# Kernel optimization log

Hardware: AMD Instinct MI355X
Metric: run time of the kernel (lower is better)

## Reference

```python
import jax, jax.numpy as jnp
import numpy as np

K_SIZE = 7
D_MODEL = 128
D_Q = 64
N_HEADS = 4
D_FF = 512
EPS = 1e-5


def _windows(x, k):
    # x: [N,E,H,W] -> [N,E,P,H,W]; zero-padded local k x k windows,
    # row-major over (dy,dx), matching nn.Unfold ordering.
    p = k // 2
    N, E, H, W = x.shape
    xp = jnp.pad(x, ((0, 0), (0, 0), (p, p), (p, p)))
    ws = [xp[:, :, i:i + H, j:j + W] for i in range(k) for j in range(k)]
    return jnp.stack(ws, axis=2)


def _layernorm(x, g, b):
    m = jnp.mean(x, -1, keepdims=True)
    v = jnp.var(x, -1, keepdims=True)
    return (x - m) * jax.lax.rsqrt(v + EPS) * g + b


def setup_inputs() -> dict:
    key = jax.random.key(0)
    ks = jax.random.split(key, 12)
    E, Q, F = D_MODEL, D_Q, D_FF

    def g(k, shape, s=0.02):
        return jax.random.normal(k, shape, jnp.float32) * s

    return dict(
        x=jax.random.normal(ks[0], (4, E, 64, 64), jnp.float32),
        qcoeff=jax.random.normal(ks[1], (4, Q), jnp.float32),
        wq=g(ks[2], (E, E)), bq=jnp.zeros((E,), jnp.float32),
        wk=g(ks[3], (E, E)), bk=jnp.zeros((E,), jnp.float32),
        wv=g(ks[4], (E, E)), bv=jnp.zeros((E,), jnp.float32),
        rel_bias=jnp.zeros((N_HEADS, K_SIZE * K_SIZE), jnp.float32),
        ln1_g=jnp.ones((E,), jnp.float32), ln1_b=jnp.zeros((E,), jnp.float32),
        bil_w=g(ks[5], (E, E, Q)), bil_b=jnp.zeros((E,), jnp.float32),
        ln2_g=jnp.ones((E,), jnp.float32), ln2_b=jnp.zeros((E,), jnp.float32),
        w1=g(ks[6], (F, E)), b1=jnp.zeros((F,), jnp.float32),
        w2=g(ks[7], (E, F)), b2=jnp.zeros((E,), jnp.float32),
    )


def reference(x, qcoeff, wq, bq, wk, bk, wv, bv, rel_bias, ln1_g, ln1_b,
              bil_w, bil_b, ln2_g, ln2_b, w1, b1, w2, b2):
    N, E, H, W = x.shape
    Nh = N_HEADS
    Hd = E // Nh
    P = K_SIZE * K_SIZE

    x_nhwc = jnp.transpose(x, (0, 2, 3, 1))              # [N,H,W,E]
    xn = _layernorm(x_nhwc, ln1_g, ln1_b)
    xnc = jnp.transpose(xn, (0, 3, 1, 2))                # [N,E,H,W]

    # 1x1-conv projections
    q = jnp.einsum('nchw,oc->nohw', xnc, wq) + bq[None, :, None, None]
    k = jnp.einsum('nchw,oc->nohw', xnc, wk) + bk[None, :, None, None]
    v = jnp.einsum('nchw,oc->nohw', xnc, wv) + bv[None, :, None, None]

    # local windows of K/V: [N,Nh,Hd,P,H,W]
    Kw = _windows(k, K_SIZE).reshape(N, Nh, Hd, P, H, W)
    Vw = _windows(v, K_SIZE).reshape(N, Nh, Hd, P, H, W)
    Qh = q.reshape(N, Nh, Hd, H, W)

    scores = jnp.einsum('nhdyx,nhdpyx->nhpyx', Qh, Kw)
    scores = scores + rel_bias[None, :, :, None, None]
    attn = jax.nn.softmax(scores, axis=2)                # softmax over P
    out = jnp.einsum('nhpyx,nhdpyx->nhdyx', attn, Vw).reshape(N, E, H, W)
    z0 = jnp.transpose(out, (0, 2, 3, 1))                # [N,H,W,E]

    # Bilinear(z0, qcoeff): qcoeff constant per (H,W) -> contract once per batch
    t = jnp.einsum('oiq,nq->noi', bil_w, qcoeff)         # [N,E,E]
    z1 = jnp.einsum('nhwi,noi->nhwo', z0, t) + bil_b

    z2 = z1 + x_nhwc
    z3 = _layernorm(z2, ln2_g, ln2_b)
    h1 = jax.nn.gelu(z3 @ w1.T + b1, approximate=False)  # dropout inactive (eval)
    z4 = h1 @ w2.T + b2 + z2
    return jnp.transpose(z4, (0, 3, 1, 2))               # [N,E,H,W]
```

## Files before the change

### kernel.cpp

```cpp
#include <hip/hip_runtime.h>
#include <cmath>

#define EPS 1e-5f
#define SZ 2097152

typedef __attribute__((ext_vector_type(8))) short short8;
typedef __attribute__((ext_vector_type(4))) float floatx4;

__device__ __forceinline__ float dot4(float4 a, float4 b) {
  return fmaf(a.x, b.x, fmaf(a.y, b.y, fmaf(a.z, b.z, a.w * b.w)));
}

__device__ __forceinline__ short f2bf(float f) {
  union { float f; unsigned u; } v; v.f = f;
  unsigned r = v.u + 0x7fff + ((v.u >> 16) & 1);
  return (short)(r >> 16);
}

__device__ __forceinline__ int xcd_band(int bid) {
  return (bid & 7) * 64 + (bid >> 3);
}

#define MFMA16(a, b, c) __builtin_amdgcn_mfma_f32_16x16x32_bf16(a, b, c, 0, 0, 0)

__global__ __launch_bounds__(512) void k_qkvln(const float* __restrict__ x,
    const float* __restrict__ g, const float* __restrict__ b,
    const float* __restrict__ wq, const float* __restrict__ wk,
    const float* __restrict__ wv, const float* __restrict__ bq,
    const float* __restrict__ bk, const float* __restrict__ bv,
    const float* __restrict__ w1, const float* __restrict__ w2,
    const float* __restrict__ bil_w, const float* __restrict__ qcoeff,
    float* __restrict__ xnhwc, short* __restrict__ qbf,
    short* __restrict__ kbf, short* __restrict__ vtb,
    short* __restrict__ w1bf, short* __restrict__ w2bf, short* __restrict__ tb) {
  __shared__ float tile[128 * 33];
  __shared__ float mres[32], rres[32];
  __shared__ __align__(16) short xs[32 * 136];
  __shared__ __align__(16) short ws[128 * 136];
  int tid = threadIdx.x;
  int l = xcd_band(blockIdx.x);
  int half = l & 1, ny = l >> 1;
  int n = ny >> 6, y = ny & 63;
  const float* xb = x + (size_t)n * 524288 + y * 64 + half * 32;
  for (int it = 0; it < 8; ++it) {
    int flat = it * 512 + tid;
    int c = flat >> 5, xpl = flat & 31;
    tile[c * 33 + xpl] = xb[(size_t)c * 4096 + xpl];
  }
  __syncthreads();
  {
    int pxl = tid >> 4, cl = tid & 15;
    float s = 0.f, sq = 0.f;
#pragma unroll
    for (int j = 0; j < 8; ++j) {
      float v = tile[(cl * 8 + j) * 33 + pxl];
      s += v; sq += v * v;
    }
    s += __shfl_xor(s, 1);  sq += __shfl_xor(sq, 1);
    s += __shfl_xor(s, 2);  sq += __shfl_xor(sq, 2);
    s += __shfl_xor(s, 4);  sq += __shfl_xor(sq, 4);
    s += __shfl_xor(s, 8);  sq += __shfl_xor(sq, 8);
    if (cl == 0) {
      float m = s * (1.f / 128.f);
      float var = sq * (1.f / 128.f) - m * m;
      mres[pxl] = m;
      rres[pxl] = rsqrtf(var + EPS);
    }
  }
  __syncthreads();
  size_t rowbase = (size_t)ny * 8192 + half * 4096;
  for (int it = 0; it < 8; ++it) {
    int flat = it * 512 + tid;
    int c = flat & 127, pxl = flat >> 7;
    float v = tile[c * 33 + pxl];
    xnhwc[rowbase + flat] = v;
    xs[pxl * 136 + c] = f2bf((v - mres[pxl]) * rres[pxl] * g[c] + b[c]);
  }
  __syncthreads();
  int w = tid >> 6, lane = tid & 63;
  int quad = lane >> 4, r16 = lane & 15;
  int wm = w & 1, wn = w >> 1;
  int stripl = wm * 16;
  short8 a[4];
#pragma unroll
  for (int kk = 0; kk < 4; ++kk)
    a[kk] = *(const short8*)&xs[(stripl + r16) * 136 + kk * 32 + quad * 8];
  const float* wptr[3] = {wq, wk, wv};
  const float* bptr[3] = {bq, bk, bv};
  for (int m = 0; m < 3; ++m) {
    __syncthreads();
    const float* wp = wptr[m];
    for (int i = tid; i < 2048; i += 512) {
      int e = i * 8;
      float4 v0 = *(const float4*)&wp[e];
      float4 v1 = *(const float4*)&wp[e + 4];
      short t8[8] = {f2bf(v0.x), f2bf(v0.y), f2bf(v0.z), f2bf(v0.w),
                     f2bf(v1.x), f2bf(v1.y), f2bf(v1.z), f2bf(v1.w)};
      int o = e >> 7, c = e & 127;
      *(uint4*)&ws[o * 136 + c] = *(uint4*)t8;
    }
    __syncthreads();
    const float* bb = bptr[m];
#pragma unroll
    for (int nt = 0; nt < 2; ++nt) {
      int o0 = wn * 32 + nt * 16;
      floatx4 acc = {0.f, 0.f, 0.f, 0.f};
#pragma unroll
      for (int kk = 0; kk < 4; ++kk) {
        short8 bfr = *(const short8*)&ws[(o0 + r16) * 136 + kk * 32 + quad * 8];
        acc = MFMA16(a[kk], bfr, acc);
      }
      float bv2 = bb[o0 + r16];
      if (m < 2) {
        short* dst = (m == 0) ? qbf : kbf;
#pragma unroll
        for (int r = 0; r < 4; ++r) {
          int pxl = stripl + quad * 4 + r;
          dst[rowbase + pxl * 128 + o0 + r16] = f2bf(acc[r] + bv2);
        }
      } else {
        short t4[4] = {f2bf(acc[0] + bv2), f2bf(acc[1] + bv2),
                       f2bf(acc[2] + bv2), f2bf(acc[3] + bv2)};
        *(uint2*)&vtb[(size_t)(n * 128 + o0 + r16) * 4096 + y * 64 + half * 32 +
                      stripl + quad * 4] = *(uint2*)t4;
      }
    }
  }
  int gtid = blockIdx.x * 512 + tid;
  if (gtid < 8192) {
    int e = gtid * 8, f = e >> 7, c = e & 127;
    float4 v0 = *(const float4*)&w1[e], v1 = *(const float4*)&w1[e + 4];
    short t8[8] = {f2bf(v0.x), f2bf(v0.y), f2bf(v0.z), f2bf(v0.w),
                   f2bf(v1.x), f2bf(v1.y), f2bf(v1.z), f2bf(v1.w)};
    *(uint4*)&w1bf[f * 136 + c] = *(uint4*)t8;
  } else if (gtid < 16384) {
    int e = (gtid - 8192) * 8, o = e >> 9, j = e & 511, ck = j >> 7, jj = j & 127;
    float4 v0 = *(const float4*)&w2[e], v1 = *(const float4*)&w2[e + 4];
    short t8[8] = {f2bf(v0.x), f2bf(v0.y), f2bf(v0.z), f2bf(v0.w),
                   f2bf(v1.x), f2bf(v1.y), f2bf(v1.z), f2bf(v1.w)};
    *(uint4*)&w2bf[(ck * 128 + o) * 136 + jj] = *(uint4*)t8;
  } else if (gtid < 81920) {
    int idx = gtid - 16384;
    int nn = idx >> 14, oi = idx & 16383;
    const float* wrow = bil_w + (size_t)oi * 64;
    const float* qc = qcoeff + nn * 64;
    float acc = 0.f;
#pragma unroll
    for (int q = 0; q < 64; q += 4) {
      float4 w4 = *(const float4*)&wrow[q];
      float4 q4 = *(const float4*)&qc[q];
      acc = fmaf(w4.x, q4.x, fmaf(w4.y, q4.y, fmaf(w4.z, q4.z, fmaf(w4.w, q4.w, acc))));
    }
    int o = oi >> 7, i = oi & 127;
    tb[nn * 17408 + o * 136 + i] = f2bf(acc);
  }
}

__global__ __launch_bounds__(512, 4) void k_at(const short* __restrict__ qbf,
    const short* __restrict__ kbf, const short* __restrict__ vtb,
    const float* __restrict__ rel_bias, const short* __restrict__ tb,
    const float* __restrict__ bil_b, const float* __restrict__ xnhwc,
    const float* __restrict__ g2, const float* __restrict__ b2ln,
    const short* __restrict__ w1bf, const float* __restrict__ b1,
    const short* __restrict__ w2bf, const float* __restrict__ b2,
    float* __restrict__ out) {
  __shared__ __align__(16) char smem[70272];
  short* h1s = (short*)smem;
  short* z3s = (short*)(smem + 44672);
  float* z2s = (float*)(smem + 53376);
  int tid = threadIdx.x;
  int l = xcd_band(blockIdx.x);
  int half = l & 1, ny = l >> 1;
  int n = ny >> 6, y = ny & 63;
  int w16 = tid >> 6, lane = tid & 63;
  int quad = lane >> 4, r16 = lane & 15;
  size_t rowbase = (size_t)ny * 8192;
  int wm = w16 & 1, wn = w16 >> 1;
  int stripL = wm * 16;
  const short* tn = tb + (size_t)n * 17408;
  float xres[2][4];
#pragma unroll
  for (int nt = 0; nt < 2; ++nt)
#pragma unroll
    for (int r = 0; r < 4; ++r)
      xres[nt][r] = xnhwc[rowbase + (half * 32 + stripL + quad * 4 + r) * 128 +
                          wn * 32 + nt * 16 + r16];
  short8 tf[2][4];
  {
    int h = w16 >> 1, swl = w16 & 1;
    int sg = half * 2 + swl;
    int strip = sg * 16;
    float* ssfw = (float*)(smem + w16 * 3200);
    short* Abw = (short*)(smem + 25600 + w16 * 2176);
    float* biasw = (float*)(smem + 43008 + w16 * 208);
    const short* qrow = qbf + (size_t)n * 524288 + (size_t)y * 8192 + h * 32;
    const short* kbp = kbf + (size_t)n * 524288 + h * 32;
    short8 qf = *(const short8*)&qrow[(strip + r16) * 128 + quad * 8];
    short8 kf[7][2];
#pragma unroll
    for (int r = 0; r < 7; ++r) {
      int yyc = min(max(y + r - 3, 0), 63);
#pragma unroll
      for (int t = 0; t < 2; ++t) {
        int gxc = min(max((sg + t) * 16 + r16 - 3, 0), 63);
        kf[r][t] = *(const short8*)&kbp[(size_t)(yyc * 64 + gxc) * 128 + quad * 8];
      }
    }
    {
      unsigned* ad = (unsigned*)Abw;
      for (int i = lane; i < 544; i += 64) ad[i] = 0u;
    }
    if (lane < 49) biasw[lane] = rel_bias[h * 49 + lane];
#pragma unroll
    for (int r = 0; r < 7; ++r) {
      bool yok = (unsigned)(y + r - 3) < 64u;
#pragma unroll
      for (int t = 0; t < 2; ++t) {
        int xxc = (sg + t) * 16 + r16;
        bool ok = yok && ((unsigned)(xxc - 3) < 64u);
        floatx4 c = MFMA16(qf, kf[r][t], ((floatx4){0.f, 0.f, 0.f, 0.f}));
#pragma unroll
        for (int rr = 0; rr < 4; ++rr) {
          int lrow = quad * 4 + rr;
          int dx = xxc - (strip + lrow);
          if ((unsigned)dx < 7u) {
            float val = ok ? c[rr] : 0.f;
            ssfw[lrow * 50 + r * 7 + dx] = val + biasw[r * 7 + dx];
          }
        }
      }
    }
    {
      int lrow = lane >> 2, sub = lane & 3;
      int p0 = sub * 12;
      float sv[13];
      float mx = -1e30f;
#pragma unroll
      for (int pi = 0; pi < 13; ++pi) {
        sv[pi] = ssfw[lrow * 50 + p0 + pi];
        mx = fmaxf(mx, sv[pi]);
      }
      mx = fmaxf(mx, __shfl_xor(mx, 1));
      mx = fmaxf(mx, __shfl_xor(mx, 2));
      float sum = 0.f;
#pragma unroll
      for (int pi = 0; pi < 13; ++pi) {
        float e = __expf(sv[pi] - mx);
        if (pi == 12 && sub != 3) e = 0.f;
        sv[pi] = e; sum += e;
      }
      sum += __shfl_xor(sum, 1);
      sum += __shfl_xor(sum, 2);
      float inv = 1.f / sum;
#pragma unroll
      for (int pi = 0; pi < 13; ++pi)
        if (pi < 12 || sub == 3) ssfw[lrow * 50 + p0 + pi] = sv[pi] * inv;
    }
    floatx4 oacc[2] = {(floatx4){0.f, 0.f, 0.f, 0.f}, (floatx4){0.f, 0.f, 0.f, 0.f}};
    int lrow = lane >> 2, sub = lane & 3;
    int pxg = strip + lrow;
    const short* vbp = vtb + (size_t)(n * 128 + h * 32) * 4096;
    short8 vf[2][2][2];
    {
      int yyc0 = min(max(y - 3, 0), 63);
#pragma unroll
      for (int kk = 0; kk < 2; ++kk)
#pragma unroll
        for (int nt = 0; nt < 2; ++nt)
          vf[0][kk][nt] = *(const short8*)&vbp[(size_t)(nt * 16 + r16) * 4096 + yyc0 * 64 + kk * 32 + quad * 8];
    }
#pragma unroll
    for (int r = 0; r < 7; ++r) {
      if (r < 6) {
        int yycn = min(max(y + r - 2, 0), 63);
#pragma unroll
        for (int kk = 0; kk < 2; ++kk)
#pragma unroll
          for (int nt = 0; nt < 2; ++nt)
            vf[(r + 1) & 1][kk][nt] = *(const short8*)&vbp[(size_t)(nt * 16 + r16) * 4096 + yycn * 64 + kk * 32 + quad * 8];
      }
      int c0 = pxg + sub - 3;
      if ((unsigned)c0 < 64u) Abw[lrow * 68 + c0] = f2bf(ssfw[lrow * 50 + r * 7 + sub]);
      int c1 = pxg + sub + 1;
      if (sub < 3 && (unsigned)c1 < 64u)
        Abw[lrow * 68 + c1] = f2bf(ssfw[lrow * 50 + r * 7 + sub + 4]);
      if ((unsigned)(y + r - 3) < 64u) {
#pragma unroll
        for (int kk = 0; kk < 2; ++kk) {
          short8 af = *(const short8*)&Abw[r16 * 68 + kk * 32 + quad * 8];
#pragma unroll
          for (int nt = 0; nt < 2; ++nt)
            oacc[nt] = MFMA16(af, vf[r & 1][kk][nt], oacc[nt]);
        }
      }
    }
#pragma unroll
    for (int nt = 0; nt < 2; ++nt)
#pragma unroll
      for (int kk = 0; kk < 4; ++kk)
        tf[nt][kk] = *(const short8*)&tn[(wn * 32 + nt * 16 + r16) * 136 + kk * 32 + quad * 8];
#pragma unroll
    for (int nt = 0; nt < 2; ++nt)
#pragma unroll
      for (int rr = 0; rr < 4; ++rr) {
        int pxl = swl * 16 + quad * 4 + rr;
        z3s[pxl * 136 + h * 32 + nt * 16 + r16] = f2bf(oacc[nt][rr]);
      }
  }
  __syncthreads();
  {
    short8 a[4];
#pragma unroll
    for (int kk = 0; kk < 4; ++kk)
      a[kk] = *(const short8*)&z3s[(stripL + r16) * 136 + kk * 32 + quad * 8];
#pragma unroll
    for (int nt = 0; nt < 2; ++nt) {
      int o0 = wn * 32 + nt * 16;
      floatx4 acc = {0.f, 0.f, 0.f, 0.f};
#pragma unroll
      for (int kk = 0; kk < 4; ++kk)
        acc = MFMA16(a[kk], tf[nt][kk], acc);
      float bb = bil_b[o0 + r16];
#pragma unroll
      for (int r = 0; r < 4; ++r) {
        int pxl = stripL + quad * 4 + r;
        z2s[pxl * 132 + o0 + r16] = acc[r] + bb + xres[nt][r];
      }
    }
  }
  __syncthreads();
  short8 wA[2][4];
#pragma unroll
  for (int nt = 0; nt < 2; ++nt)
#pragma unroll
    for (int kk = 0; kk < 4; ++kk)
      wA[nt][kk] = *(const short8*)&w1bf[(wn * 32 + nt * 16 + r16) * 136 + kk * 32 + quad * 8];
  {
    int px = tid >> 4, cl = tid & 15;
    float4 v0 = *(const float4*)&z2s[px * 132 + cl * 8];
    float4 v1 = *(const float4*)&z2s[px * 132 + cl * 8 + 4];
    float s = v0.x + v0.y + v0.z + v0.w + v1.x + v1.y + v1.z + v1.w;
    float sq = dot4(v0, v0) + dot4(v1, v1);
    s += __shfl_xor(s, 1);  sq += __shfl_xor(sq, 1);
    s += __shfl_xor(s, 2);  sq += __shfl_xor(sq, 2);
    s += __shfl_xor(s, 4);  sq += __shfl_xor(sq, 4);
    s += __shfl_xor(s, 8);  sq += __shfl_xor(sq, 8);
    float m = s * (1.f / 128.f);
    float var = sq * (1.f / 128.f) - m * m;
    float rr = rsqrtf(var + EPS);
    int c0 = cl * 8;
    short t8[8];
#pragma unroll
    for (int j = 0; j < 8; ++j) {
      float vv = (j < 4) ? (&v0.x)[j] : (&v1.x)[j - 4];
      t8[j] = f2bf((vv - m) * rr * g2[c0 + j] + b2ln[c0 + j]);
    }
    *(uint4*)&z3s[px * 136 + c0] = *(uint4*)t8;
  }
  __syncthreads();
  floatx4 zacc[2];
  zacc[0] = (floatx4){0.f, 0.f, 0.f, 0.f};
  zacc[1] = (floatx4){0.f, 0.f, 0.f, 0.f};
  for (int fc = 0; fc < 512; fc += 128) {
    short8 wB[2][4];
#pragma unroll
    for (int nt = 0; nt < 2; ++nt)
#pragma unroll
      for (int kk = 0; kk < 4; ++kk)
        wB[nt][kk] = *(const short8*)&w2bf[((fc >> 7) * 128 + wn * 32 + nt * 16 + r16) * 136 + kk * 32 + quad * 8];
    float bb1v[2];
    bb1v[0] = b1[fc + wn * 32 + r16];
    bb1v[1] = b1[fc + wn * 32 + 16 + r16];
    short8 a3[4];
#pragma unroll
    for (int kk = 0; kk < 4; ++kk)
      a3[kk] = *(const short8*)&z3s[(stripL + r16) * 136 + kk * 32 + quad * 8];
    floatx4 hacc[2];
#pragma unroll
    for (int nt = 0; nt < 2; ++nt) {
      hacc[nt] = (floatx4){0.f, 0.f, 0.f, 0.f};
#pragma unroll
      for (int kk = 0; kk < 4; ++kk)
        hacc[nt] = MFMA16(a3[kk], wA[nt][kk], hacc[nt]);
    }
    if (fc < 384) {
#pragma unroll
      for (int nt = 0; nt < 2; ++nt)
#pragma unroll
        for (int kk = 0; kk < 4; ++kk)
          wA[nt][kk] = *(const short8*)&w1bf[(fc + 128 + wn * 32 + nt * 16 + r16) * 136 + kk * 32 + quad * 8];
    }
#pragma unroll
    for (int nt = 0; nt < 2; ++nt) {
      int f0 = wn * 32 + nt * 16;
#pragma unroll
      for (int r = 0; r < 4; ++r) {
        float hv = hacc[nt][r] + bb1v[nt];
        float ge = 0.5f * hv * (1.f + erff(hv * 0.70710678118f));
        h1s[(stripL + quad * 4 + r) * 136 + f0 + r16] = f2bf(ge);
      }
    }
    __syncthreads();
    short8 ah[4];
#pragma unroll
    for (int kk = 0; kk < 4; ++kk)
      ah[kk] = *(const short8*)&h1s[(stripL + r16) * 136 + kk * 32 + quad * 8];
#pragma unroll
    for (int nt = 0; nt < 2; ++nt)
#pragma unroll
      for (int kk = 0; kk < 4; ++kk)
        zacc[nt] = MFMA16(ah[kk], wB[nt][kk], zacc[nt]);
    __syncthreads();
  }
#pragma unroll
  for (int nt = 0; nt < 2; ++nt) {
    int o = wn * 32 + nt * 16 + r16;
    float bb = b2[o];
    float res[4];
#pragma unroll
    for (int r = 0; r < 4; ++r)
      res[r] = zacc[nt][r] + bb + z2s[(stripL + quad * 4 + r) * 132 + o];
    *(float4*)&out[(((size_t)(n * 128 + o)) * 64 + y) * 64 + half * 32 + stripL + quad * 4] =
        *(float4*)res;
  }
}

extern "C" void kernel_launch(void* const* d_in, const int* in_sizes, int n_in,
                              void* d_out, int out_size, void* d_ws, size_t ws_size,
                              hipStream_t stream) {
  const float* x        = (const float*)d_in[0];
  const float* qcoeff   = (const float*)d_in[1];
  const float* wq       = (const float*)d_in[2];
  const float* bq       = (const float*)d_in[3];
  const float* wk       = (const float*)d_in[4];
  const float* bk       = (const float*)d_in[5];
  const float* wv       = (const float*)d_in[6];
  const float* bv       = (const float*)d_in[7];
  const float* rel_bias = (const float*)d_in[8];
  const float* ln1_g    = (const float*)d_in[9];
  const float* ln1_b    = (const float*)d_in[10];
  const float* bil_w    = (const float*)d_in[11];
  const float* bil_b    = (const float*)d_in[12];
  const float* ln2_g    = (const float*)d_in[13];
  const float* ln2_b    = (const float*)d_in[14];
  const float* w1       = (const float*)d_in[15];
  const float* b1       = (const float*)d_in[16];
  const float* w2       = (const float*)d_in[17];
  const float* b2       = (const float*)d_in[18];
  float* out = (float*)d_out;

  float* ws = (float*)d_ws;
  float* x_nhwc = ws;
  short* qbf = (short*)(ws + 2 * SZ);
  short* kbf = qbf + SZ;
  short* vtb = kbf + SZ;
  short* bf     = (short*)(ws + 4 * SZ);
  short* tb     = bf;
  short* w1bf   = bf + 4 * 17408;
  short* w2bf   = w1bf + 512 * 136;

  k_qkvln<<<512, 512, 0, stream>>>(x, ln1_g, ln1_b, wq, wk, wv, bq, bk, bv,
                                   w1, w2, bil_w, qcoeff,
                                   x_nhwc, qbf, kbf, vtb, w1bf, w2bf, tb);
  k_at<<<512, 512, 0, stream>>>(qbf, kbf, vtb, rel_bias, tb, bil_b, x_nhwc,
                                ln2_g, ln2_b, w1bf, b1, w2bf, b2, out);
}
```

Before: 155.3 us.

## Narrow AV MFMA K-range, double-buffer attention tile and FFN h1 buffers

```diff
diff --git a/kernel.cpp b/kernel.cpp
--- a/kernel.cpp
+++ b/kernel.cpp
@@ -164,12 +164,14 @@
     const short* __restrict__ w1bf, const float* __restrict__ b1,
     const short* __restrict__ w2bf, const float* __restrict__ b2,
     float* __restrict__ out) {
-  __shared__ __align__(16) char smem[70272];
-  short* h1s = (short*)smem;
-  short* z3s = (short*)(smem + 44672);
-  float* z2s = (float*)(smem + 53376);
+  __shared__ __align__(16) char smem[73344];
+  short* h1a = (short*)smem;
+  short* h1b = (short*)(smem + 8704);
+  short* z3s = (short*)(smem + 47744);
+  float* z2s = (float*)(smem + 56448);
   int tid = threadIdx.x;
-  int l = xcd_band(blockIdx.x);
+  int bid = blockIdx.x;
+  int l = xcd_band(bid);
   int half = l & 1, ny = l >> 1;
   int n = ny >> 6, y = ny & 63;
   int w16 = tid >> 6, lane = tid & 63;
@@ -191,8 +193,8 @@
     int sg = half * 2 + swl;
     int strip = sg * 16;
     float* ssfw = (float*)(smem + w16 * 3200);
-    short* Abw = (short*)(smem + 25600 + w16 * 2176);
-    float* biasw = (float*)(smem + 43008 + w16 * 208);
+    short* Ab = (short*)(smem + 25600 + w16 * 2560);
+    float* biasw = (float*)(smem + 46080 + w16 * 208);
     const short* qrow = qbf + (size_t)n * 524288 + (size_t)y * 8192 + h * 32;
     const short* kbp = kbf + (size_t)n * 524288 + h * 32;
     short8 qf = *(const short8*)&qrow[(strip + r16) * 128 + quad * 8];
@@ -207,8 +209,8 @@
       }
     }
     {
-      unsigned* ad = (unsigned*)Abw;
-      for (int i = lane; i < 544; i += 64) ad[i] = 0u;
+      unsigned* ad = (unsigned*)Ab;
+      for (int i = lane; i < 640; i += 64) ad[i] = 0u;
     }
     if (lane < 49) biasw[lane] = rel_bias[h * 49 + lane];
 #pragma unroll
@@ -258,40 +260,39 @@
     }
     floatx4 oacc[2] = {(floatx4){0.f, 0.f, 0.f, 0.f}, (floatx4){0.f, 0.f, 0.f, 0.f}};
     int lrow = lane >> 2, sub = lane & 3;
-    int pxg = strip + lrow;
     const short* vbp = vtb + (size_t)(n * 128 + h * 32) * 4096;
-    short8 vf[2][2][2];
+    int xa = strip + lrow + sub - 3;
+    int xb = xa + 4;
+    bool wa = (unsigned)xa < 64u;
+    bool wb = (sub < 3) && ((unsigned)xb < 64u);
+    int ka = lrow * 40 + lrow + sub + 5;
+    int kb = ka + 4;
+    long vco = (long)(strip - 8 + quad * 8);
+    if (wa) Ab[ka] = f2bf(ssfw[lrow * 50 + sub]);
+    if (wb) Ab[kb] = f2bf(ssfw[lrow * 50 + sub + 4]);
+    short8 vf[2][2];
     {
       int yyc0 = min(max(y - 3, 0), 63);
 #pragma unroll
-      for (int kk = 0; kk < 2; ++kk)
-#pragma unroll
-        for (int nt = 0; nt < 2; ++nt)
-          vf[0][kk][nt] = *(const short8*)&vbp[(size_t)(nt * 16 + r16) * 4096 + yyc0 * 64 + kk * 32 + quad * 8];
+      for (int nt = 0; nt < 2; ++nt)
+        vf[0][nt] = *(const short8*)(vbp + (long)(nt * 16 + r16) * 4096 + (long)(yyc0 * 64) + vco);
     }
 #pragma unroll
     for (int r = 0; r < 7; ++r) {
       if (r < 6) {
         int yycn = min(max(y + r - 2, 0), 63);
 #pragma unroll
-        for (int kk = 0; kk < 2; ++kk)
-#pragma unroll
-          for (int nt = 0; nt < 2; ++nt)
-            vf[(r + 1) & 1][kk][nt] = *(const short8*)&vbp[(size_t)(nt * 16 + r16) * 4096 + yycn * 64 + kk * 32 + quad * 8];
-      }
-      int c0 = pxg + sub - 3;
-      if ((unsigned)c0 < 64u) Abw[lrow * 68 + c0] = f2bf(ssfw[lrow * 50 + r * 7 + sub]);
-      int c1 = pxg + sub + 1;
-      if (sub < 3 && (unsigned)c1 < 64u)
-        Abw[lrow * 68 + c1] = f2bf(ssfw[lrow * 50 + r * 7 + sub + 4]);
+        for (int nt = 0; nt < 2; ++nt)
+          vf[(r + 1) & 1][nt] = *(const short8*)(vbp + (long)(nt * 16 + r16) * 4096 + (long)(yycn * 64) + vco);
+        short* AbN = Ab + ((r + 1) & 1) * 640;
+        if (wa) AbN[ka] = f2bf(ssfw[lrow * 50 + (r + 1) * 7 + sub]);
+        if (wb) AbN[kb] = f2bf(ssfw[lrow * 50 + (r + 1) * 7 + sub + 4]);
+      }
       if ((unsigned)(y + r - 3) < 64u) {
-#pragma unroll
-        for (int kk = 0; kk < 2; ++kk) {
-          short8 af = *(const short8*)&Abw[r16 * 68 + kk * 32 + quad * 8];
-#pragma unroll
-          for (int nt = 0; nt < 2; ++nt)
-            oacc[nt] = MFMA16(af, vf[r & 1][kk][nt], oacc[nt]);
-        }
+        short8 af = *(const short8*)&Ab[(r & 1) * 640 + r16 * 40 + quad * 8];
+#pragma unroll
+        for (int nt = 0; nt < 2; ++nt)
+          oacc[nt] = MFMA16(af, vf[r & 1][nt], oacc[nt]);
       }
     }
 #pragma unroll
@@ -329,12 +330,13 @@
     }
   }
   __syncthreads();
+  int ck0 = (bid & 1) * 2;
   short8 wA[2][4];
 #pragma unroll
   for (int nt = 0; nt < 2; ++nt)
 #pragma unroll
     for (int kk = 0; kk < 4; ++kk)
-      wA[nt][kk] = *(const short8*)&w1bf[(wn * 32 + nt * 16 + r16) * 136 + kk * 32 + quad * 8];
+      wA[nt][kk] = *(const short8*)&w1bf[(ck0 * 128 + wn * 32 + nt * 16 + r16) * 136 + kk * 32 + quad * 8];
   {
     int px = tid >> 4, cl = tid & 15;
     float4 v0 = *(const float4*)&z2s[px * 132 + cl * 8];
@@ -361,13 +363,17 @@
   floatx4 zacc[2];
   zacc[0] = (floatx4){0.f, 0.f, 0.f, 0.f};
   zacc[1] = (floatx4){0.f, 0.f, 0.f, 0.f};
-  for (int fc = 0; fc < 512; fc += 128) {
+#pragma unroll
+  for (int i = 0; i < 4; ++i) {
+    int ck = (ck0 + i) & 3;
+    int fc = ck * 128;
+    short* h1w = (i & 1) ? h1b : h1a;
     short8 wB[2][4];
 #pragma unroll
     for (int nt = 0; nt < 2; ++nt)
 #pragma unroll
       for (int kk = 0; kk < 4; ++kk)
-        wB[nt][kk] = *(const short8*)&w2bf[((fc >> 7) * 128 + wn * 32 + nt * 16 + r16) * 136 + kk * 32 + quad * 8];
+        wB[nt][kk] = *(const short8*)&w2bf[(ck * 128 + wn * 32 + nt * 16 + r16) * 136 + kk * 32 + quad * 8];
     float bb1v[2];
     bb1v[0] = b1[fc + wn * 32 + r16];
     bb1v[1] = b1[fc + wn * 32 + 16 + r16];
@@ -383,12 +389,13 @@
       for (int kk = 0; kk < 4; ++kk)
         hacc[nt] = MFMA16(a3[kk], wA[nt][kk], hacc[nt]);
     }
-    if (fc < 384) {
+    if (i < 3) {
+      int ckn = (ck0 + i + 1) & 3;
 #pragma unroll
       for (int nt = 0; nt < 2; ++nt)
 #pragma unroll
         for (int kk = 0; kk < 4; ++kk)
-          wA[nt][kk] = *(const short8*)&w1bf[(fc + 128 + wn * 32 + nt * 16 + r16) * 136 + kk * 32 + quad * 8];
+          wA[nt][kk] = *(const short8*)&w1bf[(ckn * 128 + wn * 32 + nt * 16 + r16) * 136 + kk * 32 + quad * 8];
     }
 #pragma unroll
     for (int nt = 0; nt < 2; ++nt) {
@@ -397,20 +404,19 @@
       for (int r = 0; r < 4; ++r) {
         float hv = hacc[nt][r] + bb1v[nt];
         float ge = 0.5f * hv * (1.f + erff(hv * 0.70710678118f));
-        h1s[(stripL + quad * 4 + r) * 136 + f0 + r16] = f2bf(ge);
+        h1w[(stripL + quad * 4 + r) * 136 + f0 + r16] = f2bf(ge);
       }
     }
     __syncthreads();
     short8 ah[4];
 #pragma unroll
     for (int kk = 0; kk < 4; ++kk)
-      ah[kk] = *(const short8*)&h1s[(stripL + r16) * 136 + kk * 32 + quad * 8];
+      ah[kk] = *(const short8*)&h1w[(stripL + r16) * 136 + kk * 32 + quad * 8];
 #pragma unroll
     for (int nt = 0; nt < 2; ++nt)
 #pragma unroll
       for (int kk = 0; kk < 4; ++kk)
         zacc[nt] = MFMA16(ah[kk], wB[nt][kk], zacc[nt]);
-    __syncthreads();
   }
 #pragma unroll
   for (int nt = 0; nt < 2; ++nt) {
```

After: 149.2 us. 3.9% less time.
